# Kernel optimization log

Measured on AMD Instinct MI355X. Metric: run time of the kernel, lower is better.

## Reference

```python
import jax, jax.numpy as jnp
import numpy as np

DEPTH = 16
Q_DIM = 64
V_DIM = 64
BATCH = 2048


def setup_inputs() -> dict:
    key = jax.random.key(0)
    k1, k2, k3 = jax.random.split(key, 3)
    query = jax.random.normal(k1, (BATCH, Q_DIM), dtype=jnp.float32)
    # internal-node keys: (2^depth - 1) nodes, each with 2 child keys of dim q_dim
    tree_key = jax.random.normal(k2, (2 ** DEPTH - 1, 2, Q_DIM), dtype=jnp.float32)
    # leaf values: 2^depth leaves of dim v_dim
    tree_value = jax.random.normal(k3, (2 ** DEPTH, V_DIM), dtype=jnp.float32)
    return {"query": query, "tree_key": tree_key, "tree_value": tree_value}


def _tree_attention(query, tree_key, tree_value, depth):
    # Hierarchical softmax attention over a complete binary tree.
    # At each internal node, a 2-way softmax over <query, child_key> logits
    # splits probability mass between left/right subtrees; leaf weight is the
    # product of probabilities along its root-to-leaf path.
    B = query.shape[0]
    probs = jnp.ones((B, 1), dtype=query.dtype)
    start = 0
    for d in range(depth):
        n = 2 ** d  # nodes at this level, stored contiguously at [start, start+n)
        level_keys = tree_key[start:start + n]           # (n, 2, q_dim)
        logits = jnp.einsum('bq,ncq->bnc', query, level_keys)  # (B, n, 2)
        p = jax.nn.softmax(logits, axis=-1)               # (B, n, 2)
        probs = (probs[:, :, None] * p).reshape(B, 2 * n)  # (B, 2n)
        start += n
    # weighted combination of leaf values: (B, 2^depth) @ (2^depth, v_dim)
    return probs @ tree_value


def reference(query, tree_key, tree_value):
    return _tree_attention(query, tree_key, tree_value, DEPTH)
```

## Files before the change

kernel.cpp:

```cpp
#include <hip/hip_runtime.h>

#define LOG2E 1.44269504088896f

typedef _Float16 half8  __attribute__((ext_vector_type(8)));
typedef _Float16 half4v __attribute__((ext_vector_type(4)));
typedef float    floatx4 __attribute__((ext_vector_type(4)));

#define WS_KD   0u
#define WS_VT   8388608u
#define WS_PART 16777216u

__device__ __forceinline__ floatx4 mfma16(half8 a, half8 b, floatx4 c) {
    return __builtin_amdgcn_mfma_f32_16x16x32_f16(a, b, c, 0, 0, 0);
}

__device__ __forceinline__ float sigmf(float d) {
    return __builtin_amdgcn_rcpf(1.0f + __builtin_amdgcn_exp2f(d * (-LOG2E)));
}

__device__ __forceinline__ void wave_lds_fence() {
    asm volatile("s_waitcnt lgkmcnt(0)" ::: "memory");
    __builtin_amdgcn_sched_barrier(0);
}

__global__ __launch_bounds__(256)
void k_prep(const float* __restrict__ tkey, const float* __restrict__ tval,
            char* __restrict__ ws)
{
    __shared__ _Float16 sT[64 * 72];
    const int bid = blockIdx.x, tid = threadIdx.x;

    {
        const int l = tid >> 2, part = tid & 3;
        const floatx4* vp = (const floatx4*)(tval + ((size_t)bid * 64 + l) * 64) + part * 4;
        #pragma unroll
        for (int t4 = 0; t4 < 4; ++t4) {
            floatx4 f = vp[t4];
            #pragma unroll
            for (int e = 0; e < 4; ++e)
                sT[(part * 16 + t4 * 4 + e) * 72 + l] = (_Float16)f[e];
        }
    }
    __syncthreads();
    {
        const int v = tid >> 2, q4 = tid & 3;
        half8 x0 = *(const half8*)(sT + v * 72 + 16 * q4);
        half8 x1 = *(const half8*)(sT + v * 72 + 16 * q4 + 8);
        char* base = ws + WS_VT + (size_t)bid * 8192;
        const int nt = v >> 4, lm = v & 15;
        const int u0 = 2 * q4, u1 = 2 * q4 + 1;
        *(half8*)(base + (nt * 2 + (u0 >> 2)) * 1024 + (((u0 & 3) << 4) | lm) * 16) = x0;
        *(half8*)(base + (nt * 2 + (u1 >> 2)) * 1024 + (((u1 & 3) << 4) | lm) * 16) = x1;
    }

    #pragma unroll
    for (int k = 0; k < 2; ++k) {
        const int gt  = bid * 512 + k * 256 + tid;
        const int rid = gt >> 3, part = gt & 7;
        const int s = rid >> 6, j = rid & 63;
        const size_t dst = (size_t)WS_KD + (size_t)s * 8192
                         + ((j >> 4) * 2 + (part >> 2)) * 1024
                         + (((part & 3) << 4) | (j & 15)) * 16;
        half8 out;
        if (j < 63) {
            const int u = j + 1;
            const int f = 31 - __builtin_clz(u);
            const int i = u - (1 << f);
            const int gidx = ((1 << (10 + f)) - 1) + (s << f) + i;
            const floatx4* kp = (const floatx4*)(tkey + (size_t)gidx * 128) + part * 2;
            floatx4 a0 = kp[0], a1 = kp[1];
            floatx4 b0 = kp[16], b1 = kp[17];
            #pragma unroll
            for (int e = 0; e < 4; ++e) {
                out[e]     = (_Float16)(a0[e] - b0[e]);
                out[4 + e] = (_Float16)(a1[e] - b1[e]);
            }
        } else {
            #pragma unroll
            for (int e = 0; e < 8; ++e) out[e] = (_Float16)0.f;
        }
        *(half8*)(ws + dst) = out;
    }
}

__global__ __launch_bounds__(256, 2)
void k_main(const float* __restrict__ q,
            const float* __restrict__ tkey,
            const char* __restrict__ wsc,
            _Float16* __restrict__ pout)
{
    __shared__ _Float16 sA[256 * 64];
    __shared__ _Float16 sPT[256 * 72];

    const int tid  = threadIdx.x;
    const int w    = tid >> 6;
    const int lane = tid & 63;
    const int lm   = lane & 15;
    const int quad = lane >> 4;
    const int xcd  = blockIdx.x & 7;
    const int ix   = blockIdx.x >> 3;
    const int g    = xcd * 8 + (ix >> 3);
    const int tb   = ix & 7;

    {
        const int r = tid;
        const floatx4* qp = (const floatx4*)(q + (size_t)(tb * 256 + r) * 64);
        const int sw = (r & 7) << 3;
        #pragma unroll
        for (int t4 = 0; t4 < 8; ++t4) {
            floatx4 f0 = qp[2 * t4], f1 = qp[2 * t4 + 1];
            half8 hv;
            #pragma unroll
            for (int e = 0; e < 4; ++e) { hv[e] = (_Float16)f0[e]; hv[4 + e] = (_Float16)f1[e]; }
            *(half8*)(sA + r * 64 + ((t4 * 8) ^ sw)) = hv;
        }
    }
    __syncthreads();

    half8 qA[4][2];
    #pragma unroll
    for (int m = 0; m < 4; ++m) {
        const int rA = 64 * w + 16 * m + lm;
        const int sw = (lm & 7) << 3;
        #pragma unroll
        for (int kt = 0; kt < 2; ++kt)
            qA[m][kt] = *(const half8*)(sA + rA * 64 + ((kt * 32 + quad * 8) ^ sw));
    }
    __syncthreads();

    {
        const int j = tid >> 3, part = tid & 7;
        int gidx = -1;
        if (j < 6) {
            gidx = (1 << j) - 1 + (g >> (6 - j));
        } else if (j < 21) {
            const int u = j - 5;
            const int e = 31 - __builtin_clz(u);
            const int i = u - (1 << e);
            gidx = ((1 << (6 + e)) - 1) + (g << e) + i;
        }
        half8 out;
        if (gidx >= 0) {
            const floatx4* kp = (const floatx4*)(tkey + (size_t)gidx * 128) + part * 2;
            floatx4 a0 = kp[0], a1 = kp[1];
            floatx4 b0 = kp[16], b1 = kp[17];
            #pragma unroll
            for (int e = 0; e < 4; ++e) {
                out[e]     = (_Float16)(a0[e] - b0[e]);
                out[4 + e] = (_Float16)(a1[e] - b1[e]);
            }
        } else {
            #pragma unroll
            for (int e = 0; e < 8; ++e) out[e] = (_Float16)0.f;
        }
        *(half8*)(sA + j * 64 + ((part * 8) ^ ((j & 7) << 3))) = out;
    }
    __syncthreads();

    {
        #pragma unroll
        for (int nt = 0; nt < 2; ++nt) {
            const int row = 16 * nt + lm;
            const int sw = (lm & 7) << 3;
            half8 bf0 = *(const half8*)(sA + row * 64 + ((quad * 8) ^ sw));
            half8 bf1 = *(const half8*)(sA + row * 64 + ((32 + quad * 8) ^ sw));
            floatx4 acc[4];
            #pragma unroll
            for (int m = 0; m < 4; ++m) {
                acc[m][0] = 0.f; acc[m][1] = 0.f; acc[m][2] = 0.f; acc[m][3] = 0.f;
                acc[m] = mfma16(bf0, qA[m][0], acc[m]);
                acc[m] = mfma16(bf1, qA[m][1], acc[m]);
            }
            #pragma unroll
            for (int m = 0; m < 4; ++m) {
                half4v ph;
                #pragma unroll
                for (int r = 0; r < 4; ++r) ph[r] = (_Float16)sigmf(acc[m][r]);
                *(half4v*)(sPT + (64 * w + 16 * m + lm) * 72 + 16 * nt + 4 * quad) = ph;
            }
        }
    }
    __syncthreads();

    const int bb = tid;
    float pref = 1.f;
    #pragma unroll
    for (int d = 0; d < 6; ++d) {
        float pv = (float)sPT[bb * 72 + d];
        pref *= ((g >> (5 - d)) & 1) ? (1.f - pv) : pv;
    }
    const float p6    = (float)sPT[bb * 72 + 6];
    const float p7_0  = (float)sPT[bb * 72 + 7],  p7_1  = (float)sPT[bb * 72 + 8];
    const float p9_0  = (float)sPT[bb * 72 + 9],  p9_1  = (float)sPT[bb * 72 + 10];
    const float p9_2  = (float)sPT[bb * 72 + 11], p9_3  = (float)sPT[bb * 72 + 12];
    const float p13_0 = (float)sPT[bb * 72 + 13], p13_1 = (float)sPT[bb * 72 + 14];
    const float p13_2 = (float)sPT[bb * 72 + 15], p13_3 = (float)sPT[bb * 72 + 16];
    const float p13_4 = (float)sPT[bb * 72 + 17], p13_5 = (float)sPT[bb * 72 + 18];
    const float p13_6 = (float)sPT[bb * 72 + 19], p13_7 = (float)sPT[bb * 72 + 20];

    floatx4 O[4][4];
    #pragma unroll
    for (int m = 0; m < 4; ++m)
        #pragma unroll
        for (int nt = 0; nt < 4; ++nt) { O[m][nt][0]=0.f; O[m][nt][1]=0.f; O[m][nt][2]=0.f; O[m][nt][3]=0.f; }

    for (int sl = 0; sl < 16; ++sl) {
        const int s = (g << 4) + sl;

        const char* kdp = wsc + WS_KD + (size_t)s * 8192;
        const char* vtp = wsc + WS_VT + (size_t)s * 8192;
        half8 bfr[4][2], vf[4][2];
        #pragma unroll
        for (int nt = 0; nt < 4; ++nt)
            #pragma unroll
            for (int kt = 0; kt < 2; ++kt) {
                bfr[nt][kt] = *(const half8*)(kdp + (nt * 2 + kt) * 1024 + lane * 16);
                vf[nt][kt]  = *(const half8*)(vtp + (nt * 2 + kt) * 1024 + lane * 16);
            }

        __builtin_amdgcn_s_setprio(1);
        #pragma unroll
        for (int nt = 0; nt < 4; ++nt) {
            floatx4 acc[4];
            #pragma unroll
            for (int m = 0; m < 4; ++m) {
                acc[m][0] = 0.f; acc[m][1] = 0.f; acc[m][2] = 0.f; acc[m][3] = 0.f;
                acc[m] = mfma16(bfr[nt][0], qA[m][0], acc[m]);
                acc[m] = mfma16(bfr[nt][1], qA[m][1], acc[m]);
            }
            #pragma unroll
            for (int m = 0; m < 4; ++m) {
                half4v ph;
                #pragma unroll
                for (int r = 0; r < 4; ++r) ph[r] = (_Float16)sigmf(acc[m][r]);
                *(half4v*)(sPT + (64 * w + 16 * m + lm) * 72 + 16 * nt + 4 * quad) = ph;
            }
        }
        __builtin_amdgcn_s_setprio(0);
        wave_lds_fence();

        const int a0 = sl >> 3, a1 = sl >> 2, a2 = sl >> 1;
        float P0v = pref * (a0 ? (1.f - p6) : p6);
        { float v7 = a0 ? p7_1 : p7_0;                    P0v *= (a1 & 1) ? (1.f - v7) : v7; }
        { float v9 = (a1 == 0) ? p9_0 : (a1 == 1) ? p9_1 : (a1 == 2) ? p9_2 : p9_3;
                                                          P0v *= (a2 & 1) ? (1.f - v9) : v9; }
        { float vd = (a2 == 0) ? p13_0 : (a2 == 1) ? p13_1 : (a2 == 2) ? p13_2 : (a2 == 3) ? p13_3
                   : (a2 == 4) ? p13_4 : (a2 == 5) ? p13_5 : (a2 == 6) ? p13_6 : p13_7;
                                                          P0v *= (sl & 1) ? (1.f - vd) : vd; }

        half8 pr[8];
        #pragma unroll
        for (int t = 0; t < 8; ++t)
            pr[t] = *(const half8*)(sPT + bb * 72 + t * 8);
        #define PN(n) ((float)pr[(n) >> 3][(n) & 7])

        #pragma unroll
        for (int qq = 0; qq < 4; ++qq) {
            float p0 = PN(0);
            float p1 = PN(1 + (qq >> 1));
            float P2 = P0v * (((qq >> 1) & 1) ? (1.f - p0) : p0)
                           * ((qq & 1) ? (1.f - p1) : p1);
            float p2 = PN(3 + qq);
            float A3[2]; A3[0] = P2 * p2; A3[1] = P2 * (1.f - p2);
            float A4[4];
            #pragma unroll
            for (int c = 0; c < 2; ++c) {
                float pv = PN(7 + 2 * qq + c);
                A4[2 * c] = A3[c] * pv; A4[2 * c + 1] = A3[c] * (1.f - pv);
            }
            float A5[8];
            #pragma unroll
            for (int n = 0; n < 4; ++n) {
                float pv = PN(15 + 4 * qq + n);
                A5[2 * n] = A4[n] * pv; A5[2 * n + 1] = A4[n] * (1.f - pv);
            }
            half8 lo, hi;
            #pragma unroll
            for (int n = 0; n < 8; ++n) {
                float pv = PN(31 + 8 * qq + n);
                float e0 = A5[n] * pv;
                float e1 = A5[n] * (1.f - pv);
                if (n < 4) { lo[2 * n] = (_Float16)e0; lo[2 * n + 1] = (_Float16)e1; }
                else       { hi[2 * (n - 4)] = (_Float16)e0; hi[2 * (n - 4) + 1] = (_Float16)e1; }
            }
            const int sw = (bb & 7) << 3;
            *(half8*)(sA + bb * 64 + ((16 * qq)     ^ sw)) = lo;
            *(half8*)(sA + bb * 64 + ((16 * qq + 8) ^ sw)) = hi;
        }
        #undef PN
        wave_lds_fence();

        {
            half8 af[4][2];
            #pragma unroll
            for (int m = 0; m < 4; ++m) {
                const int rA = 64 * w + 16 * m + lm;
                const int sw = (lm & 7) << 3;
                #pragma unroll
                for (int kt = 0; kt < 2; ++kt)
                    af[m][kt] = *(const half8*)(sA + rA * 64 + ((kt * 32 + quad * 8) ^ sw));
            }
            __builtin_amdgcn_s_setprio(1);
            #pragma unroll
            for (int nt = 0; nt < 4; ++nt)
                #pragma unroll
                for (int kt = 0; kt < 2; ++kt) {
                    O[0][nt] = mfma16(af[0][kt], vf[nt][kt], O[0][nt]);
                    O[1][nt] = mfma16(af[1][kt], vf[nt][kt], O[1][nt]);
                    O[2][nt] = mfma16(af[2][kt], vf[nt][kt], O[2][nt]);
                    O[3][nt] = mfma16(af[3][kt], vf[nt][kt], O[3][nt]);
                }
            __builtin_amdgcn_s_setprio(0);
        }
    }

    __syncthreads();
    #pragma unroll
    for (int m = 0; m < 4; ++m)
        #pragma unroll
        for (int nt = 0; nt < 4; ++nt)
            #pragma unroll
            for (int r = 0; r < 4; ++r) {
                const int row = 64 * w + 16 * m + 4 * quad + r;
                const int col = 16 * nt + lm;
                sA[row * 64 + (col ^ ((row & 7) << 3))] = (_Float16)O[m][nt][r];
            }
    __syncthreads();
    {
        const int row = tid;
        _Float16* dst = pout + ((size_t)g * 2048 + tb * 256 + row) * 64;
        const int sw = (row & 7) << 3;
        #pragma unroll
        for (int j = 0; j < 8; ++j)
            *(half8*)(dst + j * 8) = *(const half8*)(sA + row * 64 + ((j * 8) ^ sw));
    }
}

__global__ __launch_bounds__(256)
void k_reduce(const _Float16* __restrict__ part, float* __restrict__ outp)
{
    const int idx = blockIdx.x * 256 + threadIdx.x;
    float s0 = 0.f, s1 = 0.f, s2 = 0.f, s3 = 0.f;
    #pragma unroll 8
    for (int gg = 0; gg < 64; ++gg) {
        half4v v = *(const half4v*)(part + (size_t)gg * 131072 + (size_t)idx * 4);
        s0 += (float)v[0]; s1 += (float)v[1]; s2 += (float)v[2]; s3 += (float)v[3];
    }
    floatx4 o; o[0] = s0; o[1] = s1; o[2] = s2; o[3] = s3;
    *(floatx4*)(outp + (size_t)idx * 4) = o;
}

extern "C" void kernel_launch(void* const* d_in, const int* in_sizes, int n_in,
                              void* d_out, int out_size, void* d_ws, size_t ws_size,
                              hipStream_t stream)
{
    const float* q  = (const float*)d_in[0];
    const float* tk = (const float*)d_in[1];
    const float* tv = (const float*)d_in[2];
    float* outp = (float*)d_out;
    char*  ws   = (char*)d_ws;
    _Float16* partp = (_Float16*)(ws + WS_PART);

    k_prep  <<<dim3(1024), dim3(256), 0, stream>>>(tk, tv, ws);
    k_main  <<<dim3(512),  dim3(256), 0, stream>>>(q, tk, ws, partp);
    k_reduce<<<dim3(128),  dim3(256), 0, stream>>>(partp, outp);
}
```

Measured before the change: 164.7 us.

## Give each wave a private LDS region and drop block-wide barriers in main kernel

Replaces the two shared LDS arrays with one per-wave 64x72 region, so each wave only touches its own rows and block-wide __syncthreads become wave-local LDS fences. Query and prefix-key fragments are loaded straight from global memory into MFMA register layout instead of being staged through LDS. Total LDS per block shrinks, which could allow more resident blocks, and waves no longer wait on each other. The trade-off is redundant global loads of the key differences across waves, and the stride-72 buffer combined with the XOR swizzle changes the bank-conflict pattern.

New measurement: 167.8 us. Within noise of the previous version (+1.9%).

```diff
diff --git a/kernel.cpp b/kernel.cpp
--- a/kernel.cpp
+++ b/kernel.cpp
@@ -47,10 +47,10 @@
         half8 x0 = *(const half8*)(sT + v * 72 + 16 * q4);
         half8 x1 = *(const half8*)(sT + v * 72 + 16 * q4 + 8);
         char* base = ws + WS_VT + (size_t)bid * 8192;
-        const int nt = v >> 4, lm = v & 15;
+        const int nt = v >> 4, lmv = v & 15;
         const int u0 = 2 * q4, u1 = 2 * q4 + 1;
-        *(half8*)(base + (nt * 2 + (u0 >> 2)) * 1024 + (((u0 & 3) << 4) | lm) * 16) = x0;
-        *(half8*)(base + (nt * 2 + (u1 >> 2)) * 1024 + (((u1 & 3) << 4) | lm) * 16) = x1;
+        *(half8*)(base + (nt * 2 + (u0 >> 2)) * 1024 + (((u0 & 3) << 4) | lmv) * 16) = x0;
+        *(half8*)(base + (nt * 2 + (u1 >> 2)) * 1024 + (((u1 & 3) << 4) | lmv) * 16) = x1;
     }
 
     #pragma unroll
@@ -89,8 +89,7 @@
             const char* __restrict__ wsc,
             _Float16* __restrict__ pout)
 {
-    __shared__ _Float16 sA[256 * 64];
-    __shared__ _Float16 sPT[256 * 72];
+    __shared__ _Float16 sW[4 * 64 * 72];
 
     const int tid  = threadIdx.x;
     const int w    = tid >> 6;
@@ -102,34 +101,26 @@
     const int g    = xcd * 8 + (ix >> 3);
     const int tb   = ix & 7;
 
-    {
-        const int r = tid;
-        const floatx4* qp = (const floatx4*)(q + (size_t)(tb * 256 + r) * 64);
-        const int sw = (r & 7) << 3;
-        #pragma unroll
-        for (int t4 = 0; t4 < 8; ++t4) {
-            floatx4 f0 = qp[2 * t4], f1 = qp[2 * t4 + 1];
+    _Float16* R = sW + w * (64 * 72);
+
+    half8 qA[4][2];
+    #pragma unroll
+    for (int m = 0; m < 4; ++m)
+        #pragma unroll
+        for (int kt = 0; kt < 2; ++kt) {
+            const int row = tb * 256 + 64 * w + 16 * m + lm;
+            const floatx4* qp = (const floatx4*)(q + (size_t)row * 64 + kt * 32 + quad * 8);
+            floatx4 f0 = qp[0], f1 = qp[1];
             half8 hv;
             #pragma unroll
             for (int e = 0; e < 4; ++e) { hv[e] = (_Float16)f0[e]; hv[4 + e] = (_Float16)f1[e]; }
-            *(half8*)(sA + r * 64 + ((t4 * 8) ^ sw)) = hv;
-        }
-    }
-    __syncthreads();
-
-    half8 qA[4][2];
-    #pragma unroll
-    for (int m = 0; m < 4; ++m) {
-        const int rA = 64 * w + 16 * m + lm;
-        const int sw = (lm & 7) << 3;
-        #pragma unroll
-        for (int kt = 0; kt < 2; ++kt)
-            qA[m][kt] = *(const half8*)(sA + rA * 64 + ((kt * 32 + quad * 8) ^ sw));
-    }
-    __syncthreads();
-
-    {
-        const int j = tid >> 3, part = tid & 7;
+            qA[m][kt] = hv;
+        }
+
+    half8 pbf[2][2];
+    #pragma unroll
+    for (int nt = 0; nt < 2; ++nt) {
+        const int j = 16 * nt + lm;
         int gidx = -1;
         if (j < 6) {
             gidx = (1 << j) - 1 + (g >> (6 - j));
@@ -139,64 +130,60 @@
             const int i = u - (1 << e);
             gidx = ((1 << (6 + e)) - 1) + (g << e) + i;
         }
-        half8 out;
-        if (gidx >= 0) {
-            const floatx4* kp = (const floatx4*)(tkey + (size_t)gidx * 128) + part * 2;
-            floatx4 a0 = kp[0], a1 = kp[1];
-            floatx4 b0 = kp[16], b1 = kp[17];
-            #pragma unroll
-            for (int e = 0; e < 4; ++e) {
-                out[e]     = (_Float16)(a0[e] - b0[e]);
-                out[4 + e] = (_Float16)(a1[e] - b1[e]);
-            }
-        } else {
-            #pragma unroll
-            for (int e = 0; e < 8; ++e) out[e] = (_Float16)0.f;
-        }
-        *(half8*)(sA + j * 64 + ((part * 8) ^ ((j & 7) << 3))) = out;
-    }
-    __syncthreads();
-
-    {
-        #pragma unroll
-        for (int nt = 0; nt < 2; ++nt) {
-            const int row = 16 * nt + lm;
-            const int sw = (lm & 7) << 3;
-            half8 bf0 = *(const half8*)(sA + row * 64 + ((quad * 8) ^ sw));
-            half8 bf1 = *(const half8*)(sA + row * 64 + ((32 + quad * 8) ^ sw));
-            floatx4 acc[4];
-            #pragma unroll
-            for (int m = 0; m < 4; ++m) {
-                acc[m][0] = 0.f; acc[m][1] = 0.f; acc[m][2] = 0.f; acc[m][3] = 0.f;
-                acc[m] = mfma16(bf0, qA[m][0], acc[m]);
-                acc[m] = mfma16(bf1, qA[m][1], acc[m]);
-            }
-            #pragma unroll
-            for (int m = 0; m < 4; ++m) {
-                half4v ph;
-                #pragma unroll
-                for (int r = 0; r < 4; ++r) ph[r] = (_Float16)sigmf(acc[m][r]);
-                *(half4v*)(sPT + (64 * w + 16 * m + lm) * 72 + 16 * nt + 4 * quad) = ph;
-            }
-        }
-    }
-    __syncthreads();
-
-    const int bb = tid;
+        #pragma unroll
+        for (int kt = 0; kt < 2; ++kt) {
+            half8 out;
+            if (gidx >= 0) {
+                const floatx4* kp = (const floatx4*)(tkey + (size_t)gidx * 128 + kt * 32 + quad * 8);
+                floatx4 a0 = kp[0], a1 = kp[1];
+                floatx4 b0 = kp[16], b1 = kp[17];
+                #pragma unroll
+                for (int e = 0; e < 4; ++e) {
+                    out[e]     = (_Float16)(a0[e] - b0[e]);
+                    out[4 + e] = (_Float16)(a1[e] - b1[e]);
+                }
+            } else {
+                #pragma unroll
+                for (int e = 0; e < 8; ++e) out[e] = (_Float16)0.f;
+            }
+            pbf[nt][kt] = out;
+        }
+    }
+
+    #pragma unroll
+    for (int nt = 0; nt < 2; ++nt) {
+        floatx4 acc[4];
+        #pragma unroll
+        for (int m = 0; m < 4; ++m) {
+            acc[m][0] = 0.f; acc[m][1] = 0.f; acc[m][2] = 0.f; acc[m][3] = 0.f;
+            acc[m] = mfma16(pbf[nt][0], qA[m][0], acc[m]);
+            acc[m] = mfma16(pbf[nt][1], qA[m][1], acc[m]);
+        }
+        #pragma unroll
+        for (int m = 0; m < 4; ++m) {
+            half4v ph;
+            #pragma unroll
+            for (int r = 0; r < 4; ++r) ph[r] = (_Float16)sigmf(acc[m][r]);
+            *(half4v*)(R + (16 * m + lm) * 72 + 16 * nt + 4 * quad) = ph;
+        }
+    }
+    wave_lds_fence();
+
     float pref = 1.f;
     #pragma unroll
     for (int d = 0; d < 6; ++d) {
-        float pv = (float)sPT[bb * 72 + d];
+        float pv = (float)R[lane * 72 + d];
         pref *= ((g >> (5 - d)) & 1) ? (1.f - pv) : pv;
     }
-    const float p6    = (float)sPT[bb * 72 + 6];
-    const float p7_0  = (float)sPT[bb * 72 + 7],  p7_1  = (float)sPT[bb * 72 + 8];
-    const float p9_0  = (float)sPT[bb * 72 + 9],  p9_1  = (float)sPT[bb * 72 + 10];
-    const float p9_2  = (float)sPT[bb * 72 + 11], p9_3  = (float)sPT[bb * 72 + 12];
-    const float p13_0 = (float)sPT[bb * 72 + 13], p13_1 = (float)sPT[bb * 72 + 14];
-    const float p13_2 = (float)sPT[bb * 72 + 15], p13_3 = (float)sPT[bb * 72 + 16];
-    const float p13_4 = (float)sPT[bb * 72 + 17], p13_5 = (float)sPT[bb * 72 + 18];
-    const float p13_6 = (float)sPT[bb * 72 + 19], p13_7 = (float)sPT[bb * 72 + 20];
+    const float p6    = (float)R[lane * 72 + 6];
+    const float p7_0  = (float)R[lane * 72 + 7],  p7_1  = (float)R[lane * 72 + 8];
+    const float p9_0  = (float)R[lane * 72 + 9],  p9_1  = (float)R[lane * 72 + 10];
+    const float p9_2  = (float)R[lane * 72 + 11], p9_3  = (float)R[lane * 72 + 12];
+    const float p13_0 = (float)R[lane * 72 + 13], p13_1 = (float)R[lane * 72 + 14];
+    const float p13_2 = (float)R[lane * 72 + 15], p13_3 = (float)R[lane * 72 + 16];
+    const float p13_4 = (float)R[lane * 72 + 17], p13_5 = (float)R[lane * 72 + 18];
+    const float p13_6 = (float)R[lane * 72 + 19], p13_7 = (float)R[lane * 72 + 20];
+    wave_lds_fence();
 
     floatx4 O[4][4];
     #pragma unroll
@@ -233,7 +220,7 @@
                 half4v ph;
                 #pragma unroll
                 for (int r = 0; r < 4; ++r) ph[r] = (_Float16)sigmf(acc[m][r]);
-                *(half4v*)(sPT + (64 * w + 16 * m + lm) * 72 + 16 * nt + 4 * quad) = ph;
+                *(half4v*)(R + (16 * m + lm) * 72 + 16 * nt + 4 * quad) = ph;
             }
         }
         __builtin_amdgcn_s_setprio(0);
@@ -251,7 +238,7 @@
         half8 pr[8];
         #pragma unroll
         for (int t = 0; t < 8; ++t)
-            pr[t] = *(const half8*)(sPT + bb * 72 + t * 8);
+            pr[t] = *(const half8*)(R + lane * 72 + t * 8);
         #define PN(n) ((float)pr[(n) >> 3][(n) & 7])
 
         #pragma unroll
@@ -283,9 +270,9 @@
                 if (n < 4) { lo[2 * n] = (_Float16)e0; lo[2 * n + 1] = (_Float16)e1; }
                 else       { hi[2 * (n - 4)] = (_Float16)e0; hi[2 * (n - 4) + 1] = (_Float16)e1; }
             }
-            const int sw = (bb & 7) << 3;
-            *(half8*)(sA + bb * 64 + ((16 * qq)     ^ sw)) = lo;
-            *(half8*)(sA + bb * 64 + ((16 * qq + 8) ^ sw)) = hi;
+            const int sw = (lane & 7) << 3;
+            *(half8*)(R + lane * 72 + ((16 * qq)     ^ sw)) = lo;
+            *(half8*)(R + lane * 72 + ((16 * qq + 8) ^ sw)) = hi;
         }
         #undef PN
         wave_lds_fence();
@@ -294,11 +281,11 @@
             half8 af[4][2];
             #pragma unroll
             for (int m = 0; m < 4; ++m) {
-                const int rA = 64 * w + 16 * m + lm;
+                const int rA = 16 * m + lm;
                 const int sw = (lm & 7) << 3;
                 #pragma unroll
                 for (int kt = 0; kt < 2; ++kt)
-                    af[m][kt] = *(const half8*)(sA + rA * 64 + ((kt * 32 + quad * 8) ^ sw));
+                    af[m][kt] = *(const half8*)(R + rA * 72 + ((kt * 32 + quad * 8) ^ sw));
             }
             __builtin_amdgcn_s_setprio(1);
             #pragma unroll
@@ -314,25 +301,24 @@
         }
     }
 
-    __syncthreads();
+    wave_lds_fence();
     #pragma unroll
     for (int m = 0; m < 4; ++m)
         #pragma unroll
         for (int nt = 0; nt < 4; ++nt)
             #pragma unroll
             for (int r = 0; r < 4; ++r) {
-                const int row = 64 * w + 16 * m + 4 * quad + r;
+                const int row = 16 * m + 4 * quad + r;
                 const int col = 16 * nt + lm;
-                sA[row * 64 + (col ^ ((row & 7) << 3))] = (_Float16)O[m][nt][r];
-            }
-    __syncthreads();
+                R[row * 72 + (col ^ ((row & 7) << 3))] = (_Float16)O[m][nt][r];
+            }
+    wave_lds_fence();
     {
-        const int row = tid;
-        _Float16* dst = pout + ((size_t)g * 2048 + tb * 256 + row) * 64;
-        const int sw = (row & 7) << 3;
+        _Float16* dst = pout + ((size_t)g * 2048 + tb * 256 + 64 * w + lane) * 64;
+        const int sw = (lane & 7) << 3;
         #pragma unroll
         for (int j = 0; j < 8; ++j)
-            *(half8*)(dst + j * 8) = *(const half8*)(sA + row * 64 + ((j * 8) ^ sw));
+            *(half8*)(dst + j * 8) = *(const half8*)(R + lane * 72 + ((j * 8) ^ sw));
     }
 }
 
```
